# Kernel tuning notes

Measured on AMD Instinct MI355X. Metric: run time of the kernel, lower is better.

Reference implementation:

```python
import jax, jax.numpy as jnp
import numpy as np

V_TH = 1.0
EPS = 1e-7

# --- Poincare ball (curvature -1) exp/log maps at the origin ---
def _expmap0(v):
    n = jnp.linalg.norm(v, axis=-1, keepdims=True)
    nc = jnp.maximum(n, EPS)
    return jnp.tanh(nc) * v / nc

def _logmap0(x):
    n = jnp.linalg.norm(x, axis=-1, keepdims=True)
    nc = jnp.maximum(n, EPS)
    a = jnp.arctanh(jnp.clip(nc, EPS, 1.0 - 1e-5))
    return a * x / nc


def setup_inputs() -> dict:
    key = jax.random.key(0)
    k1, k2, k3, k4 = jax.random.split(key, 4)
    T, N, D, E = 4, 50000, 64, 800000
    s_seq = jax.random.normal(k1, (T, N, D), dtype=jnp.float32) * 0.1
    # manifold state: points inside the unit ball
    z_seq = jax.random.normal(k2, (N, D), dtype=jnp.float32) * 0.01
    W = jax.random.normal(k3, (D, D), dtype=jnp.float32) / np.sqrt(D)
    edge_index = jax.random.randint(k4, (2, E), 0, N, dtype=jnp.int64)
    return {"s_seq": s_seq, "z_seq": z_seq, "W": W, "edge_index": edge_index}


def _gcn(s_seq, W, edge_index):
    # GCNConv(channels, channels, bias=False): sym-normalized A+I, shared linear
    T, N, D = s_seq.shape
    src = jnp.concatenate([edge_index[0], jnp.arange(N, dtype=edge_index.dtype)])
    dst = jnp.concatenate([edge_index[1], jnp.arange(N, dtype=edge_index.dtype)])
    xw = jnp.einsum('tnd,kd->tnk', s_seq, W)  # lin: x @ W.T
    deg = jax.ops.segment_sum(jnp.ones_like(dst, dtype=s_seq.dtype), dst, num_segments=N)
    dinv = jnp.where(deg > 0, jax.lax.rsqrt(jnp.maximum(deg, 1.0)), 0.0)
    norm = dinv[src] * dinv[dst]                      # [E+N]
    msgs = xw[:, src, :] * norm[None, :, None]        # [T, E+N, D] gather
    agg = jax.vmap(lambda m: jax.ops.segment_sum(m, dst, num_segments=N))(msgs)
    return agg                                        # [T, N, D]


def reference(s_seq, z_seq, W, edge_index):
    x_seq = _gcn(s_seq, W, edge_index)                # [T, N, D]
    y = jnp.einsum('nd,kd->nk', x_seq.mean(0), W)     # layer.lin(x_seq.mean(0))

    # Riemannian IF neuron: per-step log->integrate->spike->soft-reset->exp
    def step(z, x_t):
        m = _logmap0(z) + x_t + y                     # charge membrane in tangent space
        o = (m >= V_TH).astype(m.dtype)               # elementwise spike
        m = m - o * V_TH                              # soft reset
        return _expmap0(m), o

    z_out, o_seq = jax.lax.scan(step, z_seq, x_seq)
    return (o_seq, z_out)
```

## Files before the change

### kernel.cpp

```cpp
#include <hip/hip_runtime.h>
#include <hip/hip_bf16.h>
#include <math.h>

static constexpr int Dd = 64;

__device__ __forceinline__ float wave_sum64(float v) {
    #pragma unroll
    for (int off = 32; off > 0; off >>= 1) v += __shfl_xor(v, off);
    return v;
}
__device__ __forceinline__ float bflo(unsigned u) { return __uint_as_float(u << 16); }
__device__ __forceinline__ float bfhi(unsigned u) { return __uint_as_float(u & 0xffff0000u); }


__global__ void deg_rank_kernel(const int* __restrict__ edst, int E,
                                int* __restrict__ deg, int* __restrict__ erank) {
    int i = blockIdx.x * blockDim.x + threadIdx.x;
    if (i < E) erank[i] = atomicAdd(&deg[edst[i]], 1);
}

__global__ void offsets_kernel(const int* __restrict__ deg, int* __restrict__ rowptr,
                               float* __restrict__ dinv, int* gctr, int N) {
    int i = blockIdx.x * blockDim.x + threadIdx.x;
    int lane = threadIdx.x & 63;
    int d = (i < N) ? deg[i] : 0;
    int incl = d;
    #pragma unroll
    for (int off = 1; off < 64; off <<= 1) {
        int u = __shfl_up(incl, off);
        if (lane >= off) incl += u;
    }
    int total = __shfl(incl, 63);
    int base = 0;
    if (lane == 0 && total > 0) base = atomicAdd(gctr, total);
    base = __shfl(base, 0);
    if (i < N) {
        rowptr[i] = base + incl - d;
        dinv[i]   = rsqrtf((float)d + 1.0f);
    }
}

__global__ void fill_pack_kernel(const int* __restrict__ esrc, const int* __restrict__ edst,
                                 const int* __restrict__ erank, const int* __restrict__ rowptr,
                                 const float* __restrict__ s, const float* __restrict__ dinv,
                                 uint2* __restrict__ sw, int* __restrict__ col,
                                 int E, int N, int fillBlocks) {
    if ((int)blockIdx.x < fillBlocks) {
        int i = blockIdx.x * 256 + threadIdx.x;
        if (i < E) col[rowptr[edst[i]] + erank[i]] = esrc[i];
    } else {
        int idx = (blockIdx.x - fillBlocks) * 256 + threadIdx.x;
        if (idx >= N * Dd) return;
        int n = idx >> 6;
        float di = dinv[n];
        size_t ND = (size_t)N * Dd;
        float v0 = s[idx] * di;
        float v1 = s[ND + idx] * di;
        float v2 = s[2 * ND + idx] * di;
        float v3 = s[3 * ND + idx] * di;
        unsigned lo = ((unsigned)__bfloat16_as_ushort(__float2bfloat16(v1)) << 16)
                    |  (unsigned)__bfloat16_as_ushort(__float2bfloat16(v0));
        unsigned hi = ((unsigned)__bfloat16_as_ushort(__float2bfloat16(v3)) << 16)
                    |  (unsigned)__bfloat16_as_ushort(__float2bfloat16(v2));
        sw[idx] = make_uint2(lo, hi);
    }
}

__global__ void __launch_bounds__(512)
fused3_kernel(const uint2* __restrict__ sw, const float* __restrict__ zin,
              const float* __restrict__ W,
              const int* __restrict__ rowptr, const int* __restrict__ deg,
              const int* __restrict__ col, const float* __restrict__ dinv,
              float* __restrict__ o_out, float* __restrict__ z_out, int N) {
    __shared__ float  WsT[Dd * 65];
    __shared__ float4 arow[8][Dd];
    __shared__ float  xms[8][Dd];

    const int tid = threadIdx.x, lane = tid & 63, wv = tid >> 6;

    for (int i = tid; i < Dd * Dd; i += 512) {
        int k = i >> 6, j = i & 63;
        WsT[j * 65 + k] = W[i];
    }
    __syncthreads();

    const int n = blockIdx.x * 8 + wv;
    const bool valid = (n < N);
    const int nn = valid ? n : (N - 1);

    const int d    = __builtin_amdgcn_readfirstlane(deg[nn]);
    const int rbeg = __builtin_amdgcn_readfirstlane(rowptr[nn]);
    const int rend = rbeg + d;
    const float din = dinv[nn];

    float2 A01 = make_float2(0.f, 0.f), A23 = make_float2(0.f, 0.f);
    #pragma unroll 8
    for (int j = rbeg; j < rend; ++j) {
        int src = col[j];
        uint2 v = sw[(size_t)src * Dd + lane];
        A01.x += bflo(v.x); A01.y += bfhi(v.x);
        A23.x += bflo(v.y); A23.y += bfhi(v.y);
    }
    {
        uint2 v = sw[(size_t)nn * Dd + lane];
        A01.x += bflo(v.x); A01.y += bfhi(v.x);
        A23.x += bflo(v.y); A23.y += bfhi(v.y);
    }
    float a0 = A01.x * din, a1 = A01.y * din, a2 = A23.x * din, a3 = A23.y * din;
    arow[wv][lane] = make_float4(a0, a1, a2, a3);

    float x0 = 0.f, x1 = 0.f, x2 = 0.f, x3 = 0.f;
    #pragma unroll 8
    for (int j = 0; j < Dd; ++j) {
        float4 b = arow[wv][j];
        float w0 = WsT[j * 65 + lane];
        x0 += b.x * w0; x1 += b.y * w0; x2 += b.z * w0; x3 += b.w * w0;
    }
    float xm = 0.25f * (x0 + x1 + x2 + x3);
    xms[wv][lane] = xm;
    float y = 0.f;
    #pragma unroll 8
    for (int j = 0; j < Dd; ++j)
        y += xms[wv][j] * WsT[j * 65 + lane];

    float z = zin[(size_t)nn * Dd + lane];
    float s2 = wave_sum64(z * z);
    float ncl = fmaxf(sqrtf(s2), 1e-7f);
    float cl = fminf(ncl, 1.0f - 1e-5f);
    float al = 0.5f * __logf((1.0f + cl) / (1.0f - cl));
    float m = (al / ncl) * z;

    float xt[4] = {x0, x1, x2, x3};
    #pragma unroll
    for (int t = 0; t < 4; ++t) {
        m += xt[t] + y;
        float o = (m >= 1.0f) ? 1.0f : 0.0f;
        if (valid) o_out[((size_t)t * N + n) * Dd + lane] = o;
        m -= o;
    }

    float s2m = wave_sum64(m * m);
    float ncm = fmaxf(sqrtf(s2m), 1e-7f);
    float e = __expf(-2.0f * ncm);
    float th = (1.0f - e) / (1.0f + e);
    if (valid) z_out[(size_t)n * Dd + lane] = (th / ncm) * m;
}


__global__ void deg_int_kernel(const int* __restrict__ edst, int E, int* __restrict__ deg) {
    int i = blockIdx.x * blockDim.x + threadIdx.x;
    if (i < E) atomicAdd(&deg[edst[i]], 1);
}

__global__ void fill_kernel(const int* __restrict__ esrc, const int* __restrict__ edst,
                            int* cursor, int* __restrict__ col, int E) {
    int i = blockIdx.x * blockDim.x + threadIdx.x;
    if (i < E) {
        int pos = atomicAdd(&cursor[edst[i]], 1);
        col[pos] = esrc[i];
    }
}

__global__ void __launch_bounds__(1024)
scan_rowptr_kernel(const int* __restrict__ deg, int* __restrict__ rowptr,
                   int* __restrict__ cursor, float* __restrict__ dinv, int N) {
    __shared__ int part[1024];
    const int tid = threadIdx.x;
    const int chunk = (N + 1023) / 1024;
    const int lo = tid * chunk;
    const int hi = min(lo + chunk, N);
    int sum = 0;
    for (int i = lo; i < hi; ++i) sum += deg[i];
    part[tid] = sum;
    __syncthreads();
    for (int off = 1; off < 1024; off <<= 1) {
        int v = (tid >= off) ? part[tid - off] : 0;
        __syncthreads();
        part[tid] += v;
        __syncthreads();
    }
    int run = (tid == 0) ? 0 : part[tid - 1];
    for (int i = lo; i < hi; ++i) {
        rowptr[i] = run;
        cursor[i] = run;
        int d = deg[i];
        dinv[i] = rsqrtf((float)d + 1.0f);
        run += d;
    }
    if (tid == 1023) rowptr[N] = part[1023];
}

__global__ void ww_kernel(const float* __restrict__ W, float* __restrict__ WW) {
    __shared__ float Ws[Dd * Dd];
    for (int i = threadIdx.x; i < Dd * Dd; i += blockDim.x) Ws[i] = W[i];
    __syncthreads();
    for (int i = threadIdx.x; i < Dd * Dd; i += blockDim.x) {
        int k = i >> 6, dcol = i & 63;
        float acc = 0.f;
        #pragma unroll
        for (int j = 0; j < Dd; ++j) acc += Ws[k * Dd + j] * Ws[j * Dd + dcol];
        WW[i] = acc;
    }
}

__global__ void __launch_bounds__(256)
fused_kernel(const float* __restrict__ s, const float* __restrict__ zin,
             const float* __restrict__ W, const float* __restrict__ WW,
             const int* __restrict__ rowptr, const int* __restrict__ col,
             const float* __restrict__ dinv,
             float* __restrict__ o_out, float* __restrict__ z_out, int N) {
    __shared__ float WsT[Dd * 65];
    __shared__ float WWsT[Dd * 65];
    __shared__ float arow[4][4][Dd];

    const int tid = threadIdx.x;
    const int lane = tid & 63;
    const int wv = tid >> 6;

    for (int i = tid; i < Dd * Dd; i += 256) {
        int k = i >> 6, j = i & 63;
        WsT[j * 65 + k]  = W[i];
        WWsT[j * 65 + k] = WW[i];
    }

    const int n = blockIdx.x * 4 + wv;
    const bool valid = (n < N);
    const int nn = valid ? n : (N - 1);

    const int rbeg = rowptr[nn];
    const int rend = rowptr[nn + 1];
    const float din = dinv[nn];
    const size_t ND = (size_t)N * Dd;

    float a0 = 0.f, a1 = 0.f, a2 = 0.f, a3 = 0.f;
    for (int base = rbeg; base < rend; base += 64) {
        int cnt = min(64, rend - base);
        int c = 0; float dv = 0.f;
        if (lane < cnt) { c = col[base + lane]; dv = dinv[c]; }
        for (int j = 0; j < cnt; ++j) {
            int src   = __shfl(c, j);
            float wgt = __shfl(dv, j);
            const float* sp = s + (size_t)src * Dd + lane;
            a0 += sp[0]      * wgt;
            a1 += sp[ND]     * wgt;
            a2 += sp[2 * ND] * wgt;
            a3 += sp[3 * ND] * wgt;
        }
    }
    {
        const float* sp = s + (size_t)nn * Dd + lane;
        float d2 = din * din;
        a0 = din * a0 + d2 * sp[0];
        a1 = din * a1 + d2 * sp[ND];
        a2 = din * a2 + d2 * sp[2 * ND];
        a3 = din * a3 + d2 * sp[3 * ND];
    }
    arow[wv][0][lane] = a0;
    arow[wv][1][lane] = a1;
    arow[wv][2][lane] = a2;
    arow[wv][3][lane] = a3;
    __syncthreads();

    float x[4] = {0.f, 0.f, 0.f, 0.f};
    float y = 0.f;
    #pragma unroll 16
    for (int j = 0; j < Dd; ++j) {
        float w0 = WsT[j * 65 + lane];
        float b0 = arow[wv][0][j], b1 = arow[wv][1][j], b2 = arow[wv][2][j], b3 = arow[wv][3][j];
        x[0] += b0 * w0; x[1] += b1 * w0; x[2] += b2 * w0; x[3] += b3 * w0;
        y += 0.25f * (b0 + b1 + b2 + b3) * WWsT[j * 65 + lane];
    }

    float z = zin[(size_t)nn * Dd + lane];
    #pragma unroll
    for (int t = 0; t < 4; ++t) {
        float s2 = wave_sum64(z * z);
        float ncl = fmaxf(sqrtf(s2), 1e-7f);
        float cl = fminf(fmaxf(ncl, 1e-7f), 1.0f - 1e-5f);
        float l = atanhf(cl) * z / ncl;
        float m = l + x[t] + y;
        float o = (m >= 1.0f) ? 1.0f : 0.0f;
        if (valid) o_out[((size_t)t * N + n) * Dd + lane] = o;
        m = m - o;
        float s2m = wave_sum64(m * m);
        float ncm = fmaxf(sqrtf(s2m), 1e-7f);
        z = tanhf(ncm) * m / ncm;
    }
    if (valid) z_out[(size_t)n * Dd + lane] = z;
}


__global__ void deg_kernel(const int* __restrict__ edst, int E, float* __restrict__ deg) {
    int i = blockIdx.x * blockDim.x + threadIdx.x;
    if (i < E) atomicAdd(&deg[edst[i]], 1.0f);
}

__global__ void dinv_kernel(const float* __restrict__ deg, float* __restrict__ dinv, int N) {
    int i = blockIdx.x * blockDim.x + threadIdx.x;
    if (i < N) dinv[i] = rsqrtf(deg[i] + 1.0f);
}

__global__ void scatter_kernel(const float* __restrict__ s,
                               const int* __restrict__ esrc,
                               const int* __restrict__ edst,
                               const float* __restrict__ dinv,
                               float* agg, int E, int N, int T) {
    int gid = blockIdx.x * blockDim.x + threadIdx.x;
    int e = gid >> 6;
    int d = gid & 63;
    if (e >= E) return;
    int src = esrc[e];
    int dst = edst[e];
    float w = dinv[src] * dinv[dst];
    #pragma unroll 4
    for (int t = 0; t < 4; ++t) {
        float v = s[((size_t)t * N + src) * Dd + d] * w;
        unsafeAtomicAdd(&agg[((size_t)t * N + dst) * Dd + d], v);
    }
}

__global__ void __launch_bounds__(256)
scan_kernel(const float* __restrict__ s, const float* __restrict__ zin,
            const float* __restrict__ W, const float* __restrict__ WW,
            const float* agg, const float* __restrict__ dinv,
            float* o_out, float* z_out, int N, int T) {
    __shared__ float WsT[Dd * 65];
    __shared__ float WWsT[Dd * 65];
    __shared__ float arow[4][4][Dd];

    const int tid = threadIdx.x;
    const int lane = tid & 63;
    const int wv = tid >> 6;

    for (int i = tid; i < Dd * Dd; i += 256) {
        int k = i >> 6, j = i & 63;
        WsT[j * 65 + k]  = W[i];
        WWsT[j * 65 + k] = WW[i];
    }

    int n = blockIdx.x * 4 + wv;
    bool valid = (n < N);
    int nn = valid ? n : (N - 1);

    float di2 = dinv[nn] * dinv[nn];
    #pragma unroll
    for (int t = 0; t < 4; ++t) {
        float v = agg[((size_t)t * N + nn) * Dd + lane]
                + s[((size_t)t * N + nn) * Dd + lane] * di2;
        arow[wv][t][lane] = v;
    }
    __syncthreads();

    float x[4] = {0.f, 0.f, 0.f, 0.f};
    float y = 0.f;
    #pragma unroll 16
    for (int j = 0; j < Dd; ++j) {
        float w0 = WsT[j * 65 + lane];
        float b0 = arow[wv][0][j], b1 = arow[wv][1][j], b2 = arow[wv][2][j], b3 = arow[wv][3][j];
        x[0] += b0 * w0; x[1] += b1 * w0; x[2] += b2 * w0; x[3] += b3 * w0;
        y += 0.25f * (b0 + b1 + b2 + b3) * WWsT[j * 65 + lane];
    }

    float z = zin[(size_t)nn * Dd + lane];
    #pragma unroll
    for (int t = 0; t < 4; ++t) {
        float s2 = wave_sum64(z * z);
        float ncl = fmaxf(sqrtf(s2), 1e-7f);
        float cl = fminf(fmaxf(ncl, 1e-7f), 1.0f - 1e-5f);
        float l = atanhf(cl) * z / ncl;
        float m = l + x[t] + y;
        float o = (m >= 1.0f) ? 1.0f : 0.0f;
        if (valid) o_out[((size_t)t * N + n) * Dd + lane] = o;
        m = m - o;
        float s2m = wave_sum64(m * m);
        float ncm = fmaxf(sqrtf(s2m), 1e-7f);
        z = tanhf(ncm) * m / ncm;
    }
    if (valid) z_out[(size_t)n * Dd + lane] = z;
}


extern "C" void kernel_launch(void* const* d_in, const int* in_sizes, int n_in,
                              void* d_out, int out_size, void* d_ws, size_t ws_size,
                              hipStream_t stream) {
    const float* s_seq = (const float*)d_in[0];
    const float* z_seq = (const float*)d_in[1];
    const float* W     = (const float*)d_in[2];
    const int*   eidx  = (const int*)d_in[3];

    const int N = in_sizes[1] / Dd;
    const int T = in_sizes[0] / in_sizes[1];
    const int E = in_sizes[3] / 2;

    const int* esrc = eidx;
    const int* edst = eidx + E;

    float* o_out = (float*)d_out;
    float* z_out = o_out + (size_t)T * N * Dd;

    size_t sw_elems = (size_t)N * Dd;
    size_t need_big = sw_elems * 8 + ((size_t)N * 3 + 1 + (size_t)E * 2) * 4 + 256;
    size_t need_mid = (size_t)N * 4 + (size_t)(N + 1) * 4 + (size_t)N * 4
                    + (size_t)E * 4 + (size_t)N * 4 + 4096 * 4;

    if (ws_size >= need_big && T == 4) {
        uint2* sw     = (uint2*)d_ws;
        int*   deg    = (int*)(sw + sw_elems);
        int*   gctr   = deg + N;
        int*   rowptr = gctr + 1;
        int*   erank  = rowptr + N;
        int*   col    = erank + E;
        float* dinv   = (float*)(col + E);

        hipMemsetAsync(deg, 0, ((size_t)N + 1) * sizeof(int), stream);
        deg_rank_kernel<<<(E + 255) / 256, 256, 0, stream>>>(edst, E, deg, erank);
        offsets_kernel<<<(N + 255) / 256, 256, 0, stream>>>(deg, rowptr, dinv, gctr, N);
        int fillBlocks = (E + 255) / 256;
        int packBlocks = (N * Dd + 255) / 256;
        fill_pack_kernel<<<fillBlocks + packBlocks, 256, 0, stream>>>(
            esrc, edst, erank, rowptr, s_seq, dinv, sw, col, E, N, fillBlocks);
        fused3_kernel<<<(N + 7) / 8, 512, 0, stream>>>(sw, z_seq, W, rowptr, deg, col,
                                                       dinv, o_out, z_out, N);
    } else if (ws_size >= need_mid) {
        int*   deg    = (int*)d_ws;
        int*   rowptr = deg + N;
        int*   cursor = rowptr + (N + 1);
        int*   col    = cursor + N;
        float* dinv   = (float*)(col + E);
        float* WW     = dinv + N;

        hipMemsetAsync(deg, 0, (size_t)N * sizeof(int), stream);
        deg_int_kernel<<<(E + 255) / 256, 256, 0, stream>>>(edst, E, deg);
        scan_rowptr_kernel<<<1, 1024, 0, stream>>>(deg, rowptr, cursor, dinv, N);
        fill_kernel<<<(E + 255) / 256, 256, 0, stream>>>(esrc, edst, cursor, col, E);
        ww_kernel<<<1, 256, 0, stream>>>(W, WW);
        fused_kernel<<<(N + 3) / 4, 256, 0, stream>>>(s_seq, z_seq, W, WW,
                                                      rowptr, col, dinv, o_out, z_out, N);
    } else {
        float* agg  = o_out;
        float* degf = (float*)d_ws;
        float* dinv = degf + N;
        float* WW   = dinv + N;

        hipMemsetAsync(agg, 0, (size_t)T * N * Dd * sizeof(float), stream);
        hipMemsetAsync(degf, 0, (size_t)N * sizeof(float), stream);
        deg_kernel<<<(E + 255) / 256, 256, 0, stream>>>(edst, E, degf);
        dinv_kernel<<<(N + 255) / 256, 256, 0, stream>>>(degf, dinv, N);
        long long threads = (long long)E * 64;
        scatter_kernel<<<(int)((threads + 255) / 256), 256, 0, stream>>>(
            s_seq, esrc, edst, dinv, agg, E, N, T);
        ww_kernel<<<1, 256, 0, stream>>>(W, WW);
        scan_kernel<<<(N + 3) / 4, 256, 0, stream>>>(s_seq, z_seq, W, WW, agg, dinv,
                                                     o_out, z_out, N, T);
    }
}
```

Measured before the change: 165.5 us.

## Move dinv scaling from packed features into per-edge CSR weights

Stops pre-scaling the packed bf16 features by the source-degree normalisation, so packing no longer depends on the degree pass and can run in the same launch as the degree/rank atomics. Each CSR entry now stores the source index together with its dinv as an int2, and the aggregation loop uses an FMA with that weight. The loop unroll is also raised. This moves feature packing off the critical path after the offsets pass, at the cost of doubling the column array size and its gather bandwidth in the main kernel.

```diff
diff --git a/kernel.cpp b/kernel.cpp
--- a/kernel.cpp
+++ b/kernel.cpp
@@ -13,10 +13,27 @@
 __device__ __forceinline__ float bfhi(unsigned u) { return __uint_as_float(u & 0xffff0000u); }
 
 
-__global__ void deg_rank_kernel(const int* __restrict__ edst, int E,
-                                int* __restrict__ deg, int* __restrict__ erank) {
-    int i = blockIdx.x * blockDim.x + threadIdx.x;
-    if (i < E) erank[i] = atomicAdd(&deg[edst[i]], 1);
+__global__ void deg_pack_kernel(const int* __restrict__ edst, int E,
+                                int* __restrict__ deg, int* __restrict__ erank,
+                                const float* __restrict__ s, uint2* __restrict__ sw,
+                                int N, int degBlocks) {
+    if ((int)blockIdx.x < degBlocks) {
+        int i = blockIdx.x * 256 + threadIdx.x;
+        if (i < E) erank[i] = atomicAdd(&deg[edst[i]], 1);
+    } else {
+        int idx = (blockIdx.x - degBlocks) * 256 + threadIdx.x;
+        if (idx >= N * Dd) return;
+        size_t ND = (size_t)N * Dd;
+        float v0 = s[idx];
+        float v1 = s[ND + idx];
+        float v2 = s[2 * ND + idx];
+        float v3 = s[3 * ND + idx];
+        unsigned lo = ((unsigned)__bfloat16_as_ushort(__float2bfloat16(v1)) << 16)
+                    |  (unsigned)__bfloat16_as_ushort(__float2bfloat16(v0));
+        unsigned hi = ((unsigned)__bfloat16_as_ushort(__float2bfloat16(v3)) << 16)
+                    |  (unsigned)__bfloat16_as_ushort(__float2bfloat16(v2));
+        sw[idx] = make_uint2(lo, hi);
+    }
 }
 
 __global__ void offsets_kernel(const int* __restrict__ deg, int* __restrict__ rowptr,
@@ -40,37 +57,22 @@
     }
 }
 
-__global__ void fill_pack_kernel(const int* __restrict__ esrc, const int* __restrict__ edst,
-                                 const int* __restrict__ erank, const int* __restrict__ rowptr,
-                                 const float* __restrict__ s, const float* __restrict__ dinv,
-                                 uint2* __restrict__ sw, int* __restrict__ col,
-                                 int E, int N, int fillBlocks) {
-    if ((int)blockIdx.x < fillBlocks) {
-        int i = blockIdx.x * 256 + threadIdx.x;
-        if (i < E) col[rowptr[edst[i]] + erank[i]] = esrc[i];
-    } else {
-        int idx = (blockIdx.x - fillBlocks) * 256 + threadIdx.x;
-        if (idx >= N * Dd) return;
-        int n = idx >> 6;
-        float di = dinv[n];
-        size_t ND = (size_t)N * Dd;
-        float v0 = s[idx] * di;
-        float v1 = s[ND + idx] * di;
-        float v2 = s[2 * ND + idx] * di;
-        float v3 = s[3 * ND + idx] * di;
-        unsigned lo = ((unsigned)__bfloat16_as_ushort(__float2bfloat16(v1)) << 16)
-                    |  (unsigned)__bfloat16_as_ushort(__float2bfloat16(v0));
-        unsigned hi = ((unsigned)__bfloat16_as_ushort(__float2bfloat16(v3)) << 16)
-                    |  (unsigned)__bfloat16_as_ushort(__float2bfloat16(v2));
-        sw[idx] = make_uint2(lo, hi);
+__global__ void fill2_kernel(const int* __restrict__ esrc, const int* __restrict__ edst,
+                             const int* __restrict__ erank, const int* __restrict__ rowptr,
+                             const float* __restrict__ dinv,
+                             int2* __restrict__ col2, int E) {
+    int i = blockIdx.x * blockDim.x + threadIdx.x;
+    if (i < E) {
+        int s = esrc[i];
+        col2[rowptr[edst[i]] + erank[i]] = make_int2(s, __float_as_int(dinv[s]));
     }
 }
 
 __global__ void __launch_bounds__(512)
-fused3_kernel(const uint2* __restrict__ sw, const float* __restrict__ zin,
+fused4_kernel(const uint2* __restrict__ sw, const float* __restrict__ zin,
               const float* __restrict__ W,
               const int* __restrict__ rowptr, const int* __restrict__ deg,
-              const int* __restrict__ col, const float* __restrict__ dinv,
+              const int2* __restrict__ col2, const float* __restrict__ dinv,
               float* __restrict__ o_out, float* __restrict__ z_out, int N) {
     __shared__ float  WsT[Dd * 65];
     __shared__ float4 arow[8][Dd];
@@ -93,20 +95,21 @@
     const int rend = rbeg + d;
     const float din = dinv[nn];
 
-    float2 A01 = make_float2(0.f, 0.f), A23 = make_float2(0.f, 0.f);
-    #pragma unroll 8
+    float a0 = 0.f, a1 = 0.f, a2 = 0.f, a3 = 0.f;
+    #pragma unroll 16
     for (int j = rbeg; j < rend; ++j) {
-        int src = col[j];
-        uint2 v = sw[(size_t)src * Dd + lane];
-        A01.x += bflo(v.x); A01.y += bfhi(v.x);
-        A23.x += bflo(v.y); A23.y += bfhi(v.y);
+        int2 cw = col2[j];
+        float w = __int_as_float(cw.y);
+        uint2 v = sw[(size_t)cw.x * Dd + lane];
+        a0 = fmaf(bflo(v.x), w, a0); a1 = fmaf(bfhi(v.x), w, a1);
+        a2 = fmaf(bflo(v.y), w, a2); a3 = fmaf(bfhi(v.y), w, a3);
     }
     {
         uint2 v = sw[(size_t)nn * Dd + lane];
-        A01.x += bflo(v.x); A01.y += bfhi(v.x);
-        A23.x += bflo(v.y); A23.y += bfhi(v.y);
-    }
-    float a0 = A01.x * din, a1 = A01.y * din, a2 = A23.x * din, a3 = A23.y * din;
+        a0 = fmaf(bflo(v.x), din, a0); a1 = fmaf(bfhi(v.x), din, a1);
+        a2 = fmaf(bflo(v.y), din, a2); a3 = fmaf(bfhi(v.y), din, a3);
+    }
+    a0 *= din; a1 *= din; a2 *= din; a3 *= din;
     arow[wv][lane] = make_float4(a0, a1, a2, a3);
 
     float x0 = 0.f, x1 = 0.f, x2 = 0.f, x3 = 0.f;
@@ -399,27 +402,29 @@
     float* z_out = o_out + (size_t)T * N * Dd;
 
     size_t sw_elems = (size_t)N * Dd;
-    size_t need_big = sw_elems * 8 + ((size_t)N * 3 + 1 + (size_t)E * 2) * 4 + 256;
+    size_t need_big = sw_elems * 8 + (size_t)E * 8
+                    + ((size_t)N * 3 + 1 + (size_t)E) * 4 + 256;
     size_t need_mid = (size_t)N * 4 + (size_t)(N + 1) * 4 + (size_t)N * 4
                     + (size_t)E * 4 + (size_t)N * 4 + 4096 * 4;
 
     if (ws_size >= need_big && T == 4) {
         uint2* sw     = (uint2*)d_ws;
-        int*   deg    = (int*)(sw + sw_elems);
+        int2*  col2   = (int2*)(sw + sw_elems);
+        int*   deg    = (int*)(col2 + E);
         int*   gctr   = deg + N;
         int*   rowptr = gctr + 1;
         int*   erank  = rowptr + N;
-        int*   col    = erank + E;
-        float* dinv   = (float*)(col + E);
+        float* dinv   = (float*)(erank + E);
 
         hipMemsetAsync(deg, 0, ((size_t)N + 1) * sizeof(int), stream);
-        deg_rank_kernel<<<(E + 255) / 256, 256, 0, stream>>>(edst, E, deg, erank);
+        int degBlocks  = (E + 255) / 256;
+        int packBlocks = (N * Dd + 255) / 256;
+        deg_pack_kernel<<<degBlocks + packBlocks, 256, 0, stream>>>(
+            edst, E, deg, erank, s_seq, sw, N, degBlocks);
         offsets_kernel<<<(N + 255) / 256, 256, 0, stream>>>(deg, rowptr, dinv, gctr, N);
-        int fillBlocks = (E + 255) / 256;
-        int packBlocks = (N * Dd + 255) / 256;
-        fill_pack_kernel<<<fillBlocks + packBlocks, 256, 0, stream>>>(
-            esrc, edst, erank, rowptr, s_seq, dinv, sw, col, E, N, fillBlocks);
-        fused3_kernel<<<(N + 7) / 8, 512, 0, stream>>>(sw, z_seq, W, rowptr, deg, col,
+        fill2_kernel<<<(E + 255) / 256, 256, 0, stream>>>(esrc, edst, erank, rowptr,
+                                                          dinv, col2, E);
+        fused4_kernel<<<(N + 7) / 8, 512, 0, stream>>>(sw, z_seq, W, rowptr, deg, col2,
                                                        dinv, o_out, z_out, N);
     } else if (ws_size >= need_mid) {
         int*   deg    = (int*)d_ws;
```

New measurement: 173.0 us. 4.5% more time.

## Use bf16 MFMA for per-node W projections in fused kernel

Applied to the files above, without the earlier changes.

Replaces the per-wave scalar FMA loops that multiply the aggregated features by W (and then by W again for y) with bf16 MFMA 16x16x32 instructions, staging W and the activations as bf16 in shared memory. It also rewrites y via linearity: the mean of the four aggregated rows is computed first, so y = W·(W·abar) and the mean moves before the projection. This cuts the LDS-bound inner-loop work and keeps the matmuls off the vector ALUs. In exchange it adds bf16 rounding of W and of intermediate activations, which can flip spike thresholds, plus extra shared-memory traffic and some wasted MFMA columns, since only 5 of 16 are used.

```diff
diff --git a/kernel.cpp b/kernel.cpp
--- a/kernel.cpp
+++ b/kernel.cpp
@@ -4,6 +4,10 @@
 
 static constexpr int Dd = 64;
 
+using s4  = __attribute__((ext_vector_type(4))) short;
+using s8  = __attribute__((ext_vector_type(8))) short;
+using f4  = __attribute__((ext_vector_type(4))) float;
+
 __device__ __forceinline__ float wave_sum64(float v) {
     #pragma unroll
     for (int off = 32; off > 0; off >>= 1) v += __shfl_xor(v, off);
@@ -11,6 +15,9 @@
 }
 __device__ __forceinline__ float bflo(unsigned u) { return __uint_as_float(u << 16); }
 __device__ __forceinline__ float bfhi(unsigned u) { return __uint_as_float(u & 0xffff0000u); }
+__device__ __forceinline__ unsigned short f2bf(float x) {
+    return __bfloat16_as_ushort(__float2bfloat16(x));
+}
 
 
 __global__ void deg_rank_kernel(const int* __restrict__ edst, int E,
@@ -58,29 +65,31 @@
         float v1 = s[ND + idx] * di;
         float v2 = s[2 * ND + idx] * di;
         float v3 = s[3 * ND + idx] * di;
-        unsigned lo = ((unsigned)__bfloat16_as_ushort(__float2bfloat16(v1)) << 16)
-                    |  (unsigned)__bfloat16_as_ushort(__float2bfloat16(v0));
-        unsigned hi = ((unsigned)__bfloat16_as_ushort(__float2bfloat16(v3)) << 16)
-                    |  (unsigned)__bfloat16_as_ushort(__float2bfloat16(v2));
+        unsigned lo = ((unsigned)f2bf(v1) << 16) | (unsigned)f2bf(v0);
+        unsigned hi = ((unsigned)f2bf(v3) << 16) | (unsigned)f2bf(v2);
         sw[idx] = make_uint2(lo, hi);
     }
 }
 
 __global__ void __launch_bounds__(512)
-fused3_kernel(const uint2* __restrict__ sw, const float* __restrict__ zin,
+fused6_kernel(const uint2* __restrict__ sw, const float* __restrict__ zin,
               const float* __restrict__ W,
               const int* __restrict__ rowptr, const int* __restrict__ deg,
               const int* __restrict__ col, const float* __restrict__ dinv,
               float* __restrict__ o_out, float* __restrict__ z_out, int N) {
-    __shared__ float  WsT[Dd * 65];
-    __shared__ float4 arow[8][Dd];
-    __shared__ float  xms[8][Dd];
+    __shared__ __align__(16) unsigned short Wb[64][68];
+    __shared__ __align__(16) unsigned short Aimg[8][16][68];
+    __shared__ float Xl[8][5][66];
 
     const int tid = threadIdx.x, lane = tid & 63, wv = tid >> 6;
 
-    for (int i = tid; i < Dd * Dd; i += 512) {
-        int k = i >> 6, j = i & 63;
-        WsT[j * 65 + k] = W[i];
+    {
+        uint2* az = (uint2*)&Aimg[0][0][0];
+        for (int i = tid; i < 2176; i += 512) az[i] = make_uint2(0u, 0u);
+    }
+    for (int i = tid; i < 64 * 64; i += 512) {
+        int r = i >> 6, k = i & 63;
+        Wb[r][k] = f2bf(W[i]);
     }
     __syncthreads();
 
@@ -107,21 +116,83 @@
         A23.x += bflo(v.y); A23.y += bfhi(v.y);
     }
     float a0 = A01.x * din, a1 = A01.y * din, a2 = A23.x * din, a3 = A23.y * din;
-    arow[wv][lane] = make_float4(a0, a1, a2, a3);
-
-    float x0 = 0.f, x1 = 0.f, x2 = 0.f, x3 = 0.f;
-    #pragma unroll 8
-    for (int j = 0; j < Dd; ++j) {
-        float4 b = arow[wv][j];
-        float w0 = WsT[j * 65 + lane];
-        x0 += b.x * w0; x1 += b.y * w0; x2 += b.z * w0; x3 += b.w * w0;
-    }
-    float xm = 0.25f * (x0 + x1 + x2 + x3);
-    xms[wv][lane] = xm;
-    float y = 0.f;
-    #pragma unroll 8
-    for (int j = 0; j < Dd; ++j)
-        y += xms[wv][j] * WsT[j * 65 + lane];
+    float abar = 0.25f * (a0 + a1 + a2 + a3);
+
+    Aimg[wv][0][lane] = f2bf(a0);
+    Aimg[wv][1][lane] = f2bf(a1);
+    Aimg[wv][2][lane] = f2bf(a2);
+    Aimg[wv][3][lane] = f2bf(a3);
+    Aimg[wv][4][lane] = f2bf(abar);
+
+    const int ncol = lane & 15;
+    const int g4   = (lane >> 4) * 4;
+
+    s8 Bf[2];
+    #pragma unroll
+    for (int ks = 0; ks < 2; ++ks) {
+        const unsigned short* bp = &Aimg[wv][ncol][ks * 32 + g4];
+        s4 lo = *(const s4*)bp;
+        s4 hi = *(const s4*)(bp + 16);
+        s8 b;
+        b[0]=lo[0]; b[1]=lo[1]; b[2]=lo[2]; b[3]=lo[3];
+        b[4]=hi[0]; b[5]=hi[1]; b[6]=hi[2]; b[7]=hi[3];
+        Bf[ks] = b;
+    }
+    #pragma unroll
+    for (int mt = 0; mt < 4; ++mt) {
+        f4 acc = {0.f, 0.f, 0.f, 0.f};
+        #pragma unroll
+        for (int ks = 0; ks < 2; ++ks) {
+            const unsigned short* ap = &Wb[mt * 16 + ncol][ks * 32 + g4];
+            s4 lo = *(const s4*)ap;
+            s4 hi = *(const s4*)(ap + 16);
+            s8 a;
+            a[0]=lo[0]; a[1]=lo[1]; a[2]=lo[2]; a[3]=lo[3];
+            a[4]=hi[0]; a[5]=hi[1]; a[6]=hi[2]; a[7]=hi[3];
+            acc = __builtin_amdgcn_mfma_f32_16x16x32_bf16(a, Bf[ks], acc, 0, 0, 0);
+        }
+        if (ncol < 5) {
+            #pragma unroll
+            for (int r = 0; r < 4; ++r)
+                Xl[wv][ncol][mt * 16 + (lane >> 4) * 4 + r] = acc[r];
+        }
+    }
+
+    float x0 = Xl[wv][0][lane], x1 = Xl[wv][1][lane];
+    float x2 = Xl[wv][2][lane], x3 = Xl[wv][3][lane];
+    float u  = Xl[wv][4][lane];
+
+    Aimg[wv][0][lane] = f2bf(u);
+    #pragma unroll
+    for (int ks = 0; ks < 2; ++ks) {
+        const unsigned short* bp = &Aimg[wv][ncol][ks * 32 + g4];
+        s4 lo = *(const s4*)bp;
+        s4 hi = *(const s4*)(bp + 16);
+        s8 b;
+        b[0]=lo[0]; b[1]=lo[1]; b[2]=lo[2]; b[3]=lo[3];
+        b[4]=hi[0]; b[5]=hi[1]; b[6]=hi[2]; b[7]=hi[3];
+        Bf[ks] = b;
+    }
+    #pragma unroll
+    for (int mt = 0; mt < 4; ++mt) {
+        f4 acc = {0.f, 0.f, 0.f, 0.f};
+        #pragma unroll
+        for (int ks = 0; ks < 2; ++ks) {
+            const unsigned short* ap = &Wb[mt * 16 + ncol][ks * 32 + g4];
+            s4 lo = *(const s4*)ap;
+            s4 hi = *(const s4*)(ap + 16);
+            s8 a;
+            a[0]=lo[0]; a[1]=lo[1]; a[2]=lo[2]; a[3]=lo[3];
+            a[4]=hi[0]; a[5]=hi[1]; a[6]=hi[2]; a[7]=hi[3];
+            acc = __builtin_amdgcn_mfma_f32_16x16x32_bf16(a, Bf[ks], acc, 0, 0, 0);
+        }
+        if (ncol == 0) {
+            #pragma unroll
+            for (int r = 0; r < 4; ++r)
+                Xl[wv][0][mt * 16 + (lane >> 4) * 4 + r] = acc[r];
+        }
+    }
+    float y = Xl[wv][0][lane];
 
     float z = zin[(size_t)nn * Dd + lane];
     float s2 = wave_sum64(z * z);
@@ -419,7 +490,7 @@
         int packBlocks = (N * Dd + 255) / 256;
         fill_pack_kernel<<<fillBlocks + packBlocks, 256, 0, stream>>>(
             esrc, edst, erank, rowptr, s_seq, dinv, sw, col, E, N, fillBlocks);
-        fused3_kernel<<<(N + 7) / 8, 512, 0, stream>>>(sw, z_seq, W, rowptr, deg, col,
+        fused6_kernel<<<(N + 7) / 8, 512, 0, stream>>>(sw, z_seq, W, rowptr, deg, col,
                                                        dinv, o_out, z_out, N);
     } else if (ws_size >= need_mid) {
         int*   deg    = (int*)d_ws;
```

Measured after the change: 155.9 us. -5.8%, faster.
